# Optimization experiments

Measured on AMD Instinct MI355X. Metric: run time of the kernel, lower is better.

Reference implementation:

```python
import jax, jax.numpy as jnp
import numpy as np

SIZE = 512
WIDTH_TILES = 1
N_STROKES = 16
STROKE_WIDTH = 0.04
N_SAMPLES = 32


def setup_inputs() -> dict:
    key = jax.random.key(0)
    # matches torch.rand(n_free,4,2)*0.6+0.2 init
    control_points = jax.random.uniform(key, (N_STROKES, 4, 2), dtype=jnp.float32) * 0.6 + 0.2
    ys = jnp.linspace(0.0, 1.0, SIZE)
    xs = jnp.linspace(0.0, 1.0, SIZE * WIDTH_TILES)
    grid_y, grid_x = jnp.meshgrid(ys, xs, indexing='ij')
    pixel_grid = jnp.stack([grid_x, grid_y], axis=-1).reshape(-1, 2).astype(jnp.float32)  # [HW,2]
    return {"control_points": control_points, "pixel_grid": pixel_grid}


def _bezier3_samples(curves):
    # curves: [S,4,2] -> [S,N_SAMPLES,2]
    ts = jnp.linspace(0.0, 1.0, N_SAMPLES, dtype=curves.dtype)
    t = ts[None, :, None]
    mt = 1.0 - t
    p0, p1, p2, p3 = (curves[:, k:k + 1, :] for k in range(4))
    return mt ** 3 * p0 + 3 * mt ** 2 * t * p1 + 3 * mt * t ** 2 * p2 + t ** 3 * p3


def reference(control_points, pixel_grid):
    pts = jnp.clip(control_points, 0.0, 1.0)  # all_strokes(), symmetric=False, no groups
    pts_flat = _bezier3_samples(pts).reshape(-1, 2)  # [P,2], P = S*N_SAMPLES
    sharpness = float(N_SAMPLES) * 8.0
    # pairwise pixel-to-sample distances: [HW,P]
    diff = pixel_grid[:, None, :] - pts_flat[None, :, :]
    dist = jnp.sqrt(jnp.sum(diff * diff, axis=-1))
    # softmin via logsumexp
    min_dist = -jax.scipy.special.logsumexp(-sharpness * dist, axis=-1) / sharpness  # [HW]
    coverage = jax.nn.sigmoid((STROKE_WIDTH - min_dist) * (8.0 / STROKE_WIDTH))
    return (1.0 - coverage).reshape(SIZE, SIZE * WIDTH_TILES)[None]  # (1,H,W)
```

## Files before the change

kernel.cpp:

```cpp
#include <hip/hip_runtime.h>


#define SIZE    512
#define NPAIRS  256
#define NGRP    64
#define MARGIN  0.05f
#define LOG2E   1.4426950408889634f
#define C2      (256.0f * LOG2E)

typedef float v2f __attribute__((ext_vector_type(2)));
typedef float v4f __attribute__((ext_vector_type(4)));

__device__ __forceinline__ float sqrt_raw(float x) { return __builtin_amdgcn_sqrtf(x); }
__device__ __forceinline__ float exp2_raw(float x) { return __builtin_amdgcn_exp2f(x); }
__device__ __forceinline__ float log2_raw(float x) { return __builtin_amdgcn_logf(x); }
__device__ __forceinline__ float rcp_raw(float x)  { return __builtin_amdgcn_rcpf(x); }
__device__ __forceinline__ float clamp01(float x)  { return fminf(fmaxf(x, 0.0f), 1.0f); }

__global__ __launch_bounds__(256) void bezier_glyph_kernel(
    const float* __restrict__ cp,
    const float* __restrict__ grid,
    float* __restrict__ out)
{
    __shared__ v4f sxy[NPAIRS];
    __shared__ v2f sp2[NPAIRS];
    __shared__ v4f sbox[NGRP];
    __shared__ v2f srep[NGRP];

    const int tid = threadIdx.x;

    {
        float px[2], py[2], pq[2];
#pragma unroll
        for (int k = 0; k < 2; ++k) {
            const int i = 2 * tid + k;
            const int stroke = i >> 5, samp = i & 31;
            const float t  = (float)samp * (1.0f / 31.0f);
            const float mt = 1.0f - t;
            const float b0 = mt * mt * mt;
            const float b1 = 3.0f * mt * mt * t;
            const float b2 = 3.0f * mt * t * t;
            const float b3 = t * t * t;
            const float* p = cp + stroke * 8;
            px[k] = b0 * clamp01(p[0]) + b1 * clamp01(p[2]) + b2 * clamp01(p[4]) + b3 * clamp01(p[6]);
            py[k] = b0 * clamp01(p[1]) + b1 * clamp01(p[3]) + b2 * clamp01(p[5]) + b3 * clamp01(p[7]);
            pq[k] = px[k] * px[k] + py[k] * py[k];
        }
        sxy[tid] = (v4f){px[0], px[1], py[0], py[1]};
        sp2[tid] = (v2f){pq[0], pq[1]};
    }
    __syncthreads();

    if (tid < NGRP) {
        float lox = 1e30f, loy = 1e30f, hix = -1e30f, hiy = -1e30f;
#pragma unroll
        for (int k = 0; k < 4; ++k) {
            const v4f a = sxy[(tid << 2) + k];
            lox = fminf(lox, fminf(a.x, a.y));
            hix = fmaxf(hix, fmaxf(a.x, a.y));
            loy = fminf(loy, fminf(a.z, a.w));
            hiy = fmaxf(hiy, fmaxf(a.z, a.w));
        }
        sbox[tid] = (v4f){lox, loy, hix, hiy};
        const v4f am = sxy[(tid << 2) + 2];
        srep[tid] = (v2f){am.x, am.z};
    }
    __syncthreads();

    const int x = (blockIdx.x << 4) + (tid & 15);
    const int y = (blockIdx.y << 4) + (tid >> 4);
    const float2 g = reinterpret_cast<const float2*>(grid)[y * SIZE + x];

    const float n2gx = -2.0f * g.x;
    const float n2gy = -2.0f * g.y;
    const float g2   = g.x * g.x + g.y * g.y;

    float ub2 = 1e30f;
#pragma unroll 8
    for (int gi = 0; gi < NGRP; ++gi) {
        const v2f r = srep[gi];
        const float dx = g.x - r.x;
        const float dy = g.y - r.y;
        ub2 = fminf(ub2, dx * dx + dy * dy);
    }
    const float tau  = sqrt_raw(ub2) + MARGIN;
    const float tau2 = tau * tau;

    unsigned long long mask = 0ull;
#pragma unroll 4
    for (int gi = 0; gi < NGRP; ++gi) {
        const v4f b = sbox[gi];
        const float dx = fmaxf(fmaxf(b.x - g.x, g.x - b.z), 0.0f);
        const float dy = fmaxf(fmaxf(b.y - g.y, g.y - b.w), 0.0f);
        const float d2 = dx * dx + dy * dy;
        if (__any(d2 < tau2)) mask |= (1ull << gi);
    }

    float m0 = 1e30f, m1 = 1e30f;
    {
        unsigned long long mm = mask;
        while (mm) {
            const int gi = __ffsll(mm) - 1;
            mm &= mm - 1;
            const int base = gi << 2;
#pragma unroll
            for (int k = 0; k < 4; ++k) {
                const v4f a = sxy[base + k];
                const v2f q = sp2[base + k];
                const v2f u = (v2f){a.x, a.y} * n2gx + ((v2f){a.z, a.w} * n2gy + q);
                m0 = fminf(m0, u.x);
                m1 = fminf(m1, u.y);
            }
        }
    }
    const float d2min = fmaxf(fminf(m0, m1) + g2, 0.0f);
    const float dmin  = sqrt_raw(d2min);
    const float bias  = C2 * dmin;

    float s0 = 0.0f, s1 = 0.0f;
    {
        unsigned long long mm = mask;
        while (mm) {
            const int gi = __ffsll(mm) - 1;
            mm &= mm - 1;
            const int base = gi << 2;
#pragma unroll
            for (int k = 0; k < 4; ++k) {
                const v4f a = sxy[base + k];
                const v2f q = sp2[base + k];
                const v2f u = (v2f){a.x, a.y} * n2gx + ((v2f){a.z, a.w} * n2gy + q);
                const float da = sqrt_raw(fmaxf(u.x + g2, 0.0f));
                const float db = sqrt_raw(fmaxf(u.y + g2, 0.0f));
                s0 += exp2_raw(__builtin_fmaf(-C2, da, bias));
                s1 += exp2_raw(__builtin_fmaf(-C2, db, bias));
            }
        }
    }
    const float s = s0 + s1;

    const float min_dist = dmin - log2_raw(s) * (1.0f / C2);
    const float z  = (0.04f - min_dist) * 200.0f;
    const float ez = exp2_raw(z * LOG2E);
    out[y * SIZE + x] = rcp_raw(1.0f + ez);
}

extern "C" void kernel_launch(void* const* d_in, const int* in_sizes, int n_in,
                              void* d_out, int out_size, void* d_ws, size_t ws_size,
                              hipStream_t stream) {
    const float* cp   = (const float*)d_in[0];
    const float* grid = (const float*)d_in[1];
    float* out = (float*)d_out;

    dim3 grid_dim(SIZE / 16, SIZE / 16);
    bezier_glyph_kernel<<<grid_dim, 256, 0, stream>>>(cp, grid, out);
}
```

Baseline: 71.72 us.

## Cull sample groups per wavefront with lane-parallel ballot and drop min-distance pass

The per-pixel loops that find the nearest representative point and test 64 bounding boxes are replaced by a per-wavefront test. Each lane handles one group against the wave's pixel rectangle, which is rebuilt from block indices assuming a uniform 1/511 grid. A shuffle reduction and a ballot then produce the shared mask. The separate pass that computed the exact minimum distance is removed, and the upper bound is used as the logsumexp stabiliser instead. This removes the culling work and one full pass over the selected samples. In exchange it relies on the grid spacing being known, and it risks exp2 overflow or lost precision when the bound is far from the true minimum.

After: 65.36 us. 1.1x faster.

```diff
diff --git a/kernel.cpp b/kernel.cpp
--- a/kernel.cpp
+++ b/kernel.cpp
@@ -67,55 +67,44 @@
     }
     __syncthreads();
 
+    const int lane = tid & 63;
+    const int wv   = tid >> 6;
     const int x = (blockIdx.x << 4) + (tid & 15);
     const int y = (blockIdx.y << 4) + (tid >> 4);
     const float2 g = reinterpret_cast<const float2*>(grid)[y * SIZE + x];
 
+    const float inv511 = 1.0f / 511.0f;
+    const float rx0 = (float)(blockIdx.x << 4) * inv511;
+    const float rx1 = (float)((blockIdx.x << 4) + 15) * inv511;
+    const float ry0 = (float)((blockIdx.y << 4) + (wv << 2)) * inv511;
+    const float ry1 = (float)((blockIdx.y << 4) + (wv << 2) + 3) * inv511;
+    const float cxr = 0.5f * (rx0 + rx1);
+    const float cyr = 0.5f * (ry0 + ry1);
+    const float hdx = 0.5f * (rx1 - rx0), hdy = 0.5f * (ry1 - ry0);
+    const float hd  = sqrt_raw(hdx * hdx + hdy * hdy);
+
+    float dc, db2;
+    {
+        const v2f r = srep[lane];
+        const float dcx = cxr - r.x, dcy = cyr - r.y;
+        dc = sqrt_raw(dcx * dcx + dcy * dcy);
+        const v4f b = sbox[lane];
+        const float bdx = fmaxf(fmaxf(b.x - rx1, rx0 - b.z), 0.0f);
+        const float bdy = fmaxf(fmaxf(b.y - ry1, ry0 - b.w), 0.0f);
+        db2 = bdx * bdx + bdy * bdy;
+    }
+    float mdc = dc;
+#pragma unroll
+    for (int s = 1; s < 64; s <<= 1) mdc = fminf(mdc, __shfl_xor(mdc, s));
+    const float ub  = mdc + hd;
+    const float tau = ub + MARGIN;
+    const unsigned long long mask = __ballot(db2 < tau * tau);
+
     const float n2gx = -2.0f * g.x;
     const float n2gy = -2.0f * g.y;
     const float g2   = g.x * g.x + g.y * g.y;
-
-    float ub2 = 1e30f;
-#pragma unroll 8
-    for (int gi = 0; gi < NGRP; ++gi) {
-        const v2f r = srep[gi];
-        const float dx = g.x - r.x;
-        const float dy = g.y - r.y;
-        ub2 = fminf(ub2, dx * dx + dy * dy);
-    }
-    const float tau  = sqrt_raw(ub2) + MARGIN;
-    const float tau2 = tau * tau;
-
-    unsigned long long mask = 0ull;
-#pragma unroll 4
-    for (int gi = 0; gi < NGRP; ++gi) {
-        const v4f b = sbox[gi];
-        const float dx = fmaxf(fmaxf(b.x - g.x, g.x - b.z), 0.0f);
-        const float dy = fmaxf(fmaxf(b.y - g.y, g.y - b.w), 0.0f);
-        const float d2 = dx * dx + dy * dy;
-        if (__any(d2 < tau2)) mask |= (1ull << gi);
-    }
-
-    float m0 = 1e30f, m1 = 1e30f;
-    {
-        unsigned long long mm = mask;
-        while (mm) {
-            const int gi = __ffsll(mm) - 1;
-            mm &= mm - 1;
-            const int base = gi << 2;
-#pragma unroll
-            for (int k = 0; k < 4; ++k) {
-                const v4f a = sxy[base + k];
-                const v2f q = sp2[base + k];
-                const v2f u = (v2f){a.x, a.y} * n2gx + ((v2f){a.z, a.w} * n2gy + q);
-                m0 = fminf(m0, u.x);
-                m1 = fminf(m1, u.y);
-            }
-        }
-    }
-    const float d2min = fmaxf(fminf(m0, m1) + g2, 0.0f);
-    const float dmin  = sqrt_raw(d2min);
-    const float bias  = C2 * dmin;
+    const v2f   g2v  = {g2, g2};
+    const float bias = C2 * ub;
 
     float s0 = 0.0f, s1 = 0.0f;
     {
@@ -129,8 +118,9 @@
                 const v4f a = sxy[base + k];
                 const v2f q = sp2[base + k];
                 const v2f u = (v2f){a.x, a.y} * n2gx + ((v2f){a.z, a.w} * n2gy + q);
-                const float da = sqrt_raw(fmaxf(u.x + g2, 0.0f));
-                const float db = sqrt_raw(fmaxf(u.y + g2, 0.0f));
+                const v2f d2v = u + g2v;
+                const float da = sqrt_raw(fmaxf(d2v.x, 0.0f));
+                const float db = sqrt_raw(fmaxf(d2v.y, 0.0f));
                 s0 += exp2_raw(__builtin_fmaf(-C2, da, bias));
                 s1 += exp2_raw(__builtin_fmaf(-C2, db, bias));
             }
@@ -138,7 +128,7 @@
     }
     const float s = s0 + s1;
 
-    const float min_dist = dmin - log2_raw(s) * (1.0f / C2);
+    const float min_dist = ub - log2_raw(s) * (1.0f / C2);
     const float z  = (0.04f - min_dist) * 200.0f;
     const float ez = exp2_raw(z * LOG2E);
     out[y * SIZE + x] = rcp_raw(1.0f + ez);
```
